# Kernel optimization log

Hardware: AMD Instinct MI355X
Metric: run time of the kernel (lower is better)

## Reference

```python
import jax, jax.numpy as jnp
import numpy as np

K_SIZE = 5
EPS = 1e-6
EPS_L = 1e-3
EPS_W = 1e-3


def setup_inputs() -> dict:
    key = jax.random.key(0)
    k1, k2, k3 = jax.random.split(key, 3)
    B, H, W = 4, 512, 512
    return {
        "input": jax.random.normal(k1, (B, 1, H, W), jnp.float32),
        "L_params": jax.random.normal(k2, (B, H, W, 3), jnp.float32),
        "w": jax.random.normal(k3, (B, 2, H, W), jnp.float32),
    }


def _bilinear(img, py, px):
    # img: (B,H,W); py,px: (B,K,H,W) absolute sample coords. Zero outside bounds
    # (matches torchvision deform_conv2d zero-padded bilinear sampling).
    B, H, W = img.shape
    y0 = jnp.floor(py)
    x0 = jnp.floor(px)
    wy = py - y0  # fractional weights
    wx = px - x0
    bidx = jnp.arange(B)[:, None, None, None]

    def corner(yc, xc, wgt):
        valid = (yc >= 0) & (yc <= H - 1) & (xc >= 0) & (xc <= W - 1)
        yi = jnp.clip(yc, 0, H - 1).astype(jnp.int32)
        xi = jnp.clip(xc, 0, W - 1).astype(jnp.int32)
        return jnp.where(valid, img[bidx, yi, xi] * wgt, 0.0)

    return (corner(y0, x0, (1 - wy) * (1 - wx))
            + corner(y0, x0 + 1, (1 - wy) * wx)
            + corner(y0 + 1, x0, wy * (1 - wx))
            + corner(y0 + 1, x0 + 1, wy * wx))


def reference(input, L_params, w):
    B, C, H, W = input.shape
    n = K_SIZE  # n_theta = ceil(sqrt(k*k)) = k

    # --- per-pixel 2x2 metric M = L L^T, L = [[a,0],[b,c]] ---
    a = jnp.abs(L_params[..., 0]) + EPS_L
    b = L_params[..., 1]
    c = jnp.abs(L_params[..., 2]) + EPS_L
    M00 = a * a            # (B,H,W)
    M01 = a * b            # = M10
    M11 = b * b + c * c

    # --- inverse of (M + eps*I), closed-form 2x2 ---
    d00 = M00 + EPS
    d11 = M11 + EPS
    det = d00 * d11 - M01 * M01
    I00 = d11 / det
    I01 = -M01 / det
    I11 = d00 / det

    # --- w rescaled so its M^{-1}-norm is < 1 (Randers condition) ---
    wx_ = w[:, 0]
    wy_ = w[:, 1]
    q = I00 * wx_ * wx_ + 2 * I01 * wx_ * wy_ + I11 * wy_ * wy_
    norm = jnp.sqrt(q + EPS)                                  # (B,H,W)
    tuned = (jax.nn.sigmoid(norm) - 0.5) * 2.0 * (1.0 - EPS_W)
    wt = w * (tuned / (norm + EPS))[:, None]                  # (B,2,H,W)

    # --- Randers unit-ball tangent sampling pattern ---
    theta = jnp.arange(0.0, 2.0 * np.pi - EPS, 2.0 * np.pi / n)  # (n,)
    ct = jnp.cos(theta)[None, :, None, None]  # (1,n,1,1)
    st = jnp.sin(theta)[None, :, None, None]
    # F(u) = sqrt(u^T M u) + <w,u>
    quad = (M00[:, None] * ct * ct + 2.0 * M01[:, None] * ct * st
            + M11[:, None] * st * st)                         # (B,n,H,W)
    F = jnp.sqrt(quad) + wt[:, 0:1] * ct + wt[:, 1:2] * st    # (B,n,H,W)
    yx = ct / (F + EPS)  # boundary point of unit Randers ball, x comp
    yy = st / (F + EPS)  # y comp

    s_interp = (jnp.arange(n, dtype=jnp.float32) + 1.0) / n   # (n,)
    s5 = s_interp[None, :, None, None, None]
    dy = (s5 * yy[:, None]).reshape(B, n * n, H, W)           # (B,K,H,W)
    dx = (s5 * yx[:, None]).reshape(B, n * n, H, W)

    gy = jnp.arange(H, dtype=jnp.float32)[None, None, :, None] + dy
    gx = jnp.arange(W, dtype=jnp.float32)[None, None, None, :] + dx

    samp = _bilinear(input[:, 0], gy, gx)                     # (B,K,H,W)
    # uniform deform-conv kernel weight 1/n^2; sample_centre=False => no centre term
    out = samp.sum(axis=1)[:, None] / float(n * n)            # (B,1,H,W)
    return out
```

## Files before the change

### kernel.cpp

```cpp
#include <hip/hip_runtime.h>
#include <math.h>

#define K_SIZE 5
#define EPS    1e-6f
#define EPS_L  1e-3f
#define EPS_W  1e-3f

#define BATCH 4
#define HGT   512
#define WID   512
#define HW    (HGT * WID)

#define ROW_ENTRIES 516
#define ROW_BYTES   (ROW_ENTRIES * 4)
#define IMG_BYTES   (HGT * ROW_BYTES)
#define TBL_BYTES   ((size_t)BATCH * IMG_BYTES)

typedef int int32x4 __attribute__((ext_vector_type(4)));
typedef _Float16 half2v __attribute__((ext_vector_type(2)));

__device__ float llvm_amdgcn_raw_buffer_load_fp32(int32x4 srsrc, int voffset,
                                                  int soffset, int aux)
    __asm("llvm.amdgcn.raw.buffer.load.f32");

__global__ __launch_bounds__(256) void pack_kernel(
    const float* __restrict__ input, char* __restrict__ tbl)
{
    const int ENT = 513;
    const int t = blockIdx.x * blockDim.x + threadIdx.x;
    if (t >= BATCH * HGT * ENT) return;
    const int k  = t % ENT;
    const int yy = (t / ENT) % HGT;
    const int b  = t / (ENT * HGT);

    const float* __restrict__ img = input + (size_t)b * HW + (size_t)yy * WID;
    const float lo = (k >= 1)   ? img[k - 1] : 0.0f;
    const float hi = (k <= 511) ? img[k]     : 0.0f;
    union { half2v h; float f; } cv;
    cv.h.x = (_Float16)lo;
    cv.h.y = (_Float16)hi;
    float* dst = (float*)(tbl + (size_t)b * IMG_BYTES + (size_t)yy * ROW_BYTES) + k;
    *dst = cv.f;
}

__global__ __launch_bounds__(256) void fused_sample_kernel_f16(
    const char* __restrict__ tbl,
    const float* __restrict__ Lp,
    const float* __restrict__ wbuf,
    float* __restrict__ out)
{
#pragma clang fp contract(off)
    const int idx = blockIdx.x * blockDim.x + threadIdx.x;

    const int b = blockIdx.x >> 10;
    const int p = idx & (HW - 1);
    const int y = p >> 9;
    const int x = p & (WID - 1);

    union {
        struct { const void* base; unsigned num; unsigned cfg; } s;
        int32x4 v;
    } desc;
    desc.s.base = (const void*)(tbl + (size_t)b * IMG_BYTES);
    desc.s.num  = (unsigned)IMG_BYTES;
    desc.s.cfg  = 0x00020000u;
    const int32x4 rsrc = desc.v;

    const size_t l_off = (size_t)idx * 3;
    const float L0 = Lp[l_off + 0];
    const float L1 = Lp[l_off + 1];
    const float L2 = Lp[l_off + 2];

    const float a  = fabsf(L0) + EPS_L;
    const float bb = L1;
    const float c  = fabsf(L2) + EPS_L;

    const float M00 = a * a;
    const float M01 = a * bb;
    const float M11 = (bb * bb) + (c * c);

    const float d00 = M00 + EPS;
    const float d11 = M11 + EPS;
    const float det = (d00 * d11) - (M01 * M01);
    const float I00 = d11 / det;
    const float I01 = (-M01) / det;
    const float I11 = d00 / det;

    const float wx = wbuf[(size_t)b * 2 * HW + p];
    const float wy = wbuf[(size_t)b * 2 * HW + HW + p];

    const float q    = (((I00 * wx) * wx) + (((2.0f * I01) * wx) * wy)) + ((I11 * wy) * wy);
    const float norm = sqrtf(q + EPS);

    const float e    = (float)exp((double)(-norm));
    const float sig  = 1.0f / (1.0f + e);
    const float tuned = ((sig - 0.5f) * 2.0f) * (1.0f - EPS_W);
    const float scale = tuned / (norm + EPS);
    const float wtx = wx * scale;
    const float wty = wy * scale;

    const float CT[K_SIZE] = { 1.0f,  0.30901696090f, -0.80901703575f, -0.80901693229f,  0.30901712828f };
    const float ST[K_SIZE] = { 0.0f,  0.95105652717f,  0.58778519534f, -0.58778533774f, -0.95105647279f };
    const float SV[K_SIZE] = { 0.2f, 0.4f, 0.6f, 0.8f, 1.0f };

    const float fy = (float)y;
    const float fx = (float)x;

    float acc0 = 0.0f;
    float acc1 = 0.0f;

    #pragma unroll
    for (int k = 0; k < K_SIZE; ++k) {
        const float ct = CT[k];
        const float st = ST[k];
        const float quad = (((M00 * ct) * ct) + (((2.0f * M01) * ct) * st)) + ((M11 * st) * st);
        const float F    = (sqrtf(quad) + (wtx * ct)) + (wty * st);
        const float Fe   = F + EPS;
        const float rFe  = __builtin_amdgcn_rcpf(Fe);
        const float yx   = ct * rFe;
        const float yy   = st * rFe;

        #pragma unroll
        for (int s = 0; s < K_SIZE; ++s) {
            const float sv = SV[s];
            const float gy = fmaf(sv, yy, fy);
            const float gx = fmaf(sv, yx, fx);

            const int   y0i = (int)floorf(gy);
            const int   x0i = (int)floorf(gx);
            const float wyf = __builtin_amdgcn_fractf(gy);
            const float wxf = __builtin_amdgcn_fractf(gx);

            const int   ke  = min(max(x0i + 1, 0), 512);
            const unsigned r0   = (unsigned)y0i * (unsigned)ROW_BYTES;
            const unsigned off0 = r0 + ((unsigned)ke << 2);
            const unsigned off1 = off0 + (unsigned)ROW_BYTES;

            const float p0f = llvm_amdgcn_raw_buffer_load_fp32(rsrc, (int)off0, 0, 0);
            const float p1f = llvm_amdgcn_raw_buffer_load_fp32(rsrc, (int)off1, 0, 0);

            union { float f; half2v h; } c0, c1;
            c0.f = p0f;
            c1.f = p1f;
            const float v00 = (float)c0.h.x;
            const float v01 = (float)c0.h.y;
            const float v10 = (float)c1.h.x;
            const float v11 = (float)c1.h.y;

            const int x1i = x0i + 1;
            const bool vx0 = (unsigned)x0i < (unsigned)WID;
            const bool vx1 = (unsigned)x1i < (unsigned)WID;
            const float zx0 = vx0 ? (1.0f - wxf) : 0.0f;
            const float zx1 = vx1 ? wxf : 0.0f;

            const float row0 = fmaf(v01, zx1, v00 * zx0);
            const float row1 = fmaf(v11, zx1, v10 * zx0);

            if (s & 1) {
                acc1 = fmaf(1.0f - wyf, row0, acc1);
                acc1 = fmaf(wyf,        row1, acc1);
            } else {
                acc0 = fmaf(1.0f - wyf, row0, acc0);
                acc0 = fmaf(wyf,        row1, acc0);
            }
        }
    }

    out[idx] = (acc0 + acc1) / (float)(K_SIZE * K_SIZE);
}

__global__ __launch_bounds__(256) void fused_sample_kernel_f32(
    const float* __restrict__ input,
    const float* __restrict__ Lp,
    const float* __restrict__ wbuf,
    float* __restrict__ out)
{
#pragma clang fp contract(off)
    const int idx = blockIdx.x * blockDim.x + threadIdx.x;
    const int b = blockIdx.x >> 10;
    const int p = idx & (HW - 1);
    const int y = p >> 9;
    const int x = p & (WID - 1);

    union {
        struct { const void* base; unsigned num; unsigned cfg; } s;
        int32x4 v;
    } desc;
    desc.s.base = (const void*)(input + (size_t)b * HW);
    desc.s.num  = HW * 4u;
    desc.s.cfg  = 0x00020000u;
    const int32x4 rsrc = desc.v;

    const size_t l_off = (size_t)idx * 3;
    const float L0 = Lp[l_off + 0];
    const float L1 = Lp[l_off + 1];
    const float L2 = Lp[l_off + 2];

    const float a  = fabsf(L0) + EPS_L;
    const float bb = L1;
    const float c  = fabsf(L2) + EPS_L;

    const float M00 = a * a;
    const float M01 = a * bb;
    const float M11 = (bb * bb) + (c * c);

    const float d00 = M00 + EPS;
    const float d11 = M11 + EPS;
    const float det = (d00 * d11) - (M01 * M01);
    const float I00 = d11 / det;
    const float I01 = (-M01) / det;
    const float I11 = d00 / det;

    const float wx = wbuf[(size_t)b * 2 * HW + p];
    const float wy = wbuf[(size_t)b * 2 * HW + HW + p];

    const float q    = (((I00 * wx) * wx) + (((2.0f * I01) * wx) * wy)) + ((I11 * wy) * wy);
    const float norm = sqrtf(q + EPS);
    const float e    = (float)exp((double)(-norm));
    const float sig  = 1.0f / (1.0f + e);
    const float tuned = ((sig - 0.5f) * 2.0f) * (1.0f - EPS_W);
    const float scale = tuned / (norm + EPS);
    const float wtx = wx * scale;
    const float wty = wy * scale;

    const float CT[K_SIZE] = { 1.0f,  0.30901696090f, -0.80901703575f, -0.80901693229f,  0.30901712828f };
    const float ST[K_SIZE] = { 0.0f,  0.95105652717f,  0.58778519534f, -0.58778533774f, -0.95105647279f };
    const float SV[K_SIZE] = { 0.2f, 0.4f, 0.6f, 0.8f, 1.0f };

    const float fy = (float)y;
    const float fx = (float)x;

    float acc0 = 0.0f;
    float acc1 = 0.0f;

    #pragma unroll
    for (int k = 0; k < K_SIZE; ++k) {
        const float ct = CT[k];
        const float st = ST[k];
        const float quad = (((M00 * ct) * ct) + (((2.0f * M01) * ct) * st)) + ((M11 * st) * st);
        const float F    = (sqrtf(quad) + (wtx * ct)) + (wty * st);
        const float Fe   = F + EPS;
        const float rFe  = __builtin_amdgcn_rcpf(Fe);
        const float yx   = ct * rFe;
        const float yy   = st * rFe;

        #pragma unroll
        for (int s = 0; s < K_SIZE; ++s) {
            const float sv = SV[s];
            const float gy = fmaf(sv, yy, fy);
            const float gx = fmaf(sv, yx, fx);

            const int   y0i = (int)floorf(gy);
            const int   x0i = (int)floorf(gx);
            const float wyf = __builtin_amdgcn_fractf(gy);
            const float wxf = __builtin_amdgcn_fractf(gx);

            const unsigned r0 = (unsigned)y0i << 11;
            const unsigned r1 = r0 + (WID * 4u);

            const int x1i = x0i + 1;
            const bool vx0 = (unsigned)x0i < (unsigned)WID;
            const bool vx1 = (unsigned)x1i < (unsigned)WID;
            const unsigned x0v = (unsigned)min(max(x0i, 0), WID - 1) << 2;
            const unsigned x1v = (unsigned)min(max(x1i, 0), WID - 1) << 2;

            const float v00 = llvm_amdgcn_raw_buffer_load_fp32(rsrc, (int)(r0 + x0v), 0, 0);
            const float v01 = llvm_amdgcn_raw_buffer_load_fp32(rsrc, (int)(r0 + x1v), 0, 0);
            const float v10 = llvm_amdgcn_raw_buffer_load_fp32(rsrc, (int)(r1 + x0v), 0, 0);
            const float v11 = llvm_amdgcn_raw_buffer_load_fp32(rsrc, (int)(r1 + x1v), 0, 0);

            const float zx0 = vx0 ? (1.0f - wxf) : 0.0f;
            const float zx1 = vx1 ? wxf : 0.0f;

            const float row0 = fmaf(v01, zx1, v00 * zx0);
            const float row1 = fmaf(v11, zx1, v10 * zx0);

            if (s & 1) {
                acc1 = fmaf(1.0f - wyf, row0, acc1);
                acc1 = fmaf(wyf,        row1, acc1);
            } else {
                acc0 = fmaf(1.0f - wyf, row0, acc0);
                acc0 = fmaf(wyf,        row1, acc0);
            }
        }
    }

    out[idx] = (acc0 + acc1) / (float)(K_SIZE * K_SIZE);
}

extern "C" void kernel_launch(void* const* d_in, const int* in_sizes, int n_in,
                              void* d_out, int out_size, void* d_ws, size_t ws_size,
                              hipStream_t stream) {
    const float* input = (const float*)d_in[0];
    const float* Lp    = (const float*)d_in[1];
    const float* wbuf  = (const float*)d_in[2];
    float* out = (float*)d_out;

    if (ws_size >= TBL_BYTES) {
        char* tbl = (char*)d_ws;
        const int pack_total = BATCH * HGT * 513;
        pack_kernel<<<(pack_total + 255) / 256, 256, 0, stream>>>(input, tbl);
        fused_sample_kernel_f16<<<BATCH * HW / 256, 256, 0, stream>>>(tbl, Lp, wbuf, out);
    } else {
        fused_sample_kernel_f32<<<BATCH * HW / 256, 256, 0, stream>>>(input, Lp, wbuf, out);
    }
}
```

Baseline: 42.87 us.

## Pack 2x2 bilinear neighborhoods into one 8-byte f16 entry per sample

The packed table now stores all four bilinear corners (top and bottom rows, left and right columns) as four halves in one 8-byte entry, with zero padding built in at the image borders. Each sample in the fused kernel then issues one 64-bit buffer load instead of two 32-bit loads, which halves the gather instruction count. In exchange the table doubles in size, so the pack kernel writes more and the gathers use more cache footprint. The pack kernel also reads each input pixel four times.

```diff
diff --git a/kernel.cpp b/kernel.cpp
--- a/kernel.cpp
+++ b/kernel.cpp
@@ -11,35 +11,47 @@
 #define WID   512
 #define HW    (HGT * WID)
 
-#define ROW_ENTRIES 516
-#define ROW_BYTES   (ROW_ENTRIES * 4)
-#define IMG_BYTES   (HGT * ROW_BYTES)
-#define TBL_BYTES   ((size_t)BATCH * IMG_BYTES)
+#define ENT        513
+#define ROW_ENTRIES 520
+#define ROW_BYTES  (ROW_ENTRIES * 8)
+#define IMG_BYTES  (ENT * ROW_BYTES)
+#define TBL_BYTES  ((size_t)BATCH * IMG_BYTES)
 
 typedef int int32x4 __attribute__((ext_vector_type(4)));
+typedef float floatx2 __attribute__((ext_vector_type(2)));
+typedef _Float16 half4v __attribute__((ext_vector_type(4)));
 typedef _Float16 half2v __attribute__((ext_vector_type(2)));
 
 __device__ float llvm_amdgcn_raw_buffer_load_fp32(int32x4 srsrc, int voffset,
                                                   int soffset, int aux)
     __asm("llvm.amdgcn.raw.buffer.load.f32");
+__device__ floatx2 llvm_amdgcn_raw_buffer_load_2fp32(int32x4 srsrc, int voffset,
+                                                     int soffset, int aux)
+    __asm("llvm.amdgcn.raw.buffer.load.v2f32");
 
 __global__ __launch_bounds__(256) void pack_kernel(
     const float* __restrict__ input, char* __restrict__ tbl)
 {
-    const int ENT = 513;
     const int t = blockIdx.x * blockDim.x + threadIdx.x;
-    if (t >= BATCH * HGT * ENT) return;
+    if (t >= BATCH * ENT * ENT) return;
     const int k  = t % ENT;
-    const int yy = (t / ENT) % HGT;
-    const int b  = t / (ENT * HGT);
-
-    const float* __restrict__ img = input + (size_t)b * HW + (size_t)yy * WID;
-    const float lo = (k >= 1)   ? img[k - 1] : 0.0f;
-    const float hi = (k <= 511) ? img[k]     : 0.0f;
-    union { half2v h; float f; } cv;
-    cv.h.x = (_Float16)lo;
-    cv.h.y = (_Float16)hi;
-    float* dst = (float*)(tbl + (size_t)b * IMG_BYTES + (size_t)yy * ROW_BYTES) + k;
+    const int ri = (t / ENT) % ENT;
+    const int b  = t / (ENT * ENT);
+
+    const float* __restrict__ img = input + (size_t)b * HW;
+
+    const bool top = (ri >= 1), bot = (ri <= HGT - 1);
+    const bool lef = (k  >= 1), rig = (k  <= WID - 1);
+    const int yT = (ri - 1) << 9;
+    const int yB = ri << 9;
+
+    union { half4v h; floatx2 f; } cv;
+    cv.h.x = (_Float16)((top && lef) ? img[yT + k - 1] : 0.0f);
+    cv.h.y = (_Float16)((top && rig) ? img[yT + k]     : 0.0f);
+    cv.h.z = (_Float16)((bot && lef) ? img[yB + k - 1] : 0.0f);
+    cv.h.w = (_Float16)((bot && rig) ? img[yB + k]     : 0.0f);
+
+    floatx2* dst = (floatx2*)(tbl + (size_t)b * IMG_BYTES + (size_t)ri * ROW_BYTES + ((size_t)k << 3));
     *dst = cv.f;
 }
 
@@ -131,25 +143,20 @@
             const float wyf = __builtin_amdgcn_fractf(gy);
             const float wxf = __builtin_amdgcn_fractf(gx);
 
-            const int   ke  = min(max(x0i + 1, 0), 512);
-            const unsigned r0   = (unsigned)y0i * (unsigned)ROW_BYTES;
-            const unsigned off0 = r0 + ((unsigned)ke << 2);
-            const unsigned off1 = off0 + (unsigned)ROW_BYTES;
-
-            const float p0f = llvm_amdgcn_raw_buffer_load_fp32(rsrc, (int)off0, 0, 0);
-            const float p1f = llvm_amdgcn_raw_buffer_load_fp32(rsrc, (int)off1, 0, 0);
-
-            union { float f; half2v h; } c0, c1;
-            c0.f = p0f;
-            c1.f = p1f;
-            const float v00 = (float)c0.h.x;
-            const float v01 = (float)c0.h.y;
-            const float v10 = (float)c1.h.x;
-            const float v11 = (float)c1.h.y;
-
-            const int x1i = x0i + 1;
+            const int ri = y0i + 1;
+            const int ke = min(max(x0i + 1, 0), ENT - 1);
+            const unsigned off = (unsigned)ri * (unsigned)ROW_BYTES + ((unsigned)ke << 3);
+
+            const floatx2 pf = llvm_amdgcn_raw_buffer_load_2fp32(rsrc, (int)off, 0, 0);
+            union { floatx2 f; half4v h; } cv;
+            cv.f = pf;
+            const float v00 = (float)cv.h.x;
+            const float v01 = (float)cv.h.y;
+            const float v10 = (float)cv.h.z;
+            const float v11 = (float)cv.h.w;
+
             const bool vx0 = (unsigned)x0i < (unsigned)WID;
-            const bool vx1 = (unsigned)x1i < (unsigned)WID;
+            const bool vx1 = (unsigned)(x0i + 1) < (unsigned)WID;
             const float zx0 = vx0 ? (1.0f - wxf) : 0.0f;
             const float zx1 = vx1 ? wxf : 0.0f;
 
@@ -298,7 +305,7 @@
 
     if (ws_size >= TBL_BYTES) {
         char* tbl = (char*)d_ws;
-        const int pack_total = BATCH * HGT * 513;
+        const int pack_total = BATCH * ENT * ENT;
         pack_kernel<<<(pack_total + 255) / 256, 256, 0, stream>>>(input, tbl);
         fused_sample_kernel_f16<<<BATCH * HW / 256, 256, 0, stream>>>(tbl, Lp, wbuf, out);
     } else {
```

New measurement: 39.86 us. 7.0% less time.
